# Kernel tuning notes

Hardware: AMD Instinct MI355X
Metric: run time of the kernel (lower is better)

## Reference

```python
import jax, jax.numpy as jnp
import numpy as np

N_NODES = 50000
N_EDGES = 800000
IN_FEATURES = 256
HIDDEN = 128


def setup_inputs() -> dict:
    key = jax.random.key(0)
    k_x, k_r, k_c, k_v, k_w, k_b = jax.random.split(key, 6)
    x = jax.random.normal(k_x, (N_NODES, IN_FEATURES), dtype=jnp.float32)
    adj_row = jax.random.randint(k_r, (N_EDGES,), 0, N_NODES, dtype=jnp.int32)
    adj_col = jax.random.randint(k_c, (N_EDGES,), 0, N_NODES, dtype=jnp.int32)
    adj_val = jax.random.uniform(k_v, (N_EDGES,), dtype=jnp.float32)
    # Linear params: weight [hidden, in_features] (xavier-normal-ish), bias [hidden]
    std = float(np.sqrt(2.0 / (IN_FEATURES + HIDDEN)))
    W = jax.random.normal(k_w, (HIDDEN, IN_FEATURES), dtype=jnp.float32) * std
    b = jax.random.normal(k_b, (HIDDEN,), dtype=jnp.float32) * 0.01
    return {"x": x, "adj_row": adj_row, "adj_col": adj_col, "adj_val": adj_val, "W": W, "b": b}


def reference(x, adj_row, adj_col, adj_val, W, b):
    # support = Linear(x): [N, hidden]
    support = jnp.einsum('nf,hf->nh', x, W) + b
    # sparse adj @ support via edge-list gather + segment-sum scatter
    gathered = support[adj_col] * adj_val[:, None]          # [E, hidden]
    out = jax.ops.segment_sum(gathered, adj_row, num_segments=N_NODES)  # [N, hidden]
    return out
```

## Files before the change

kernel.cpp:

```cpp
#include <hip/hip_runtime.h>

#define N_NODES 50000
#define N_EDGES 800000
#define IN_F    256
#define HIDDEN  128

#define BUCKET_SZ 64
#define NB        782
#define NBINS     1024
#define EBLOCK    3328
#define EPT       13
#define EBLOCKS   241
#define LIN_ROWS  64
#define LBLOCKS   782
#define NTASKS    1023
#define OFST_W    256
#define CAP       1300
#define NFRAG     4096

#define SMEM_BYTES 35840

typedef __attribute__((ext_vector_type(8))) short bf16x8;
typedef __attribute__((ext_vector_type(4))) float f32x4;

__device__ inline unsigned short f2bf(float f) {
    unsigned u = __float_as_uint(f);
    u += 0x7FFF + ((u >> 16) & 1);
    return (unsigned short)(u >> 16);
}
__device__ inline bf16x8 cvt8(float4 a, float4 b) {
    bf16x8 r;
    r[0] = (short)f2bf(a.x); r[1] = (short)f2bf(a.y);
    r[2] = (short)f2bf(a.z); r[3] = (short)f2bf(a.w);
    r[4] = (short)f2bf(b.x); r[5] = (short)f2bf(b.y);
    r[6] = (short)f2bf(b.z); r[7] = (short)f2bf(b.w);
    return r;
}
__device__ inline float bfLo(unsigned u) { return __uint_as_float(u << 16); }
__device__ inline float bfHi(unsigned u) { return __uint_as_float(u & 0xFFFF0000u); }

__global__ __launch_bounds__(256) void wconv_kernel(
    const float* __restrict__ W, unsigned short* __restrict__ wb)
{
    const int f = blockIdx.x * 256 + threadIdx.x;
    if (f >= NFRAG) return;
    const int ln = f & 63;
    const int s  = (f >> 6) & 7;
    const int hk = f >> 9;
    const int row = s * 16 + (ln & 15);
    const int k0  = hk * 32 + (ln >> 4) * 8;
    const float* wp = W + (size_t)row * IN_F + k0;
    float4 b0 = *(const float4*)wp;
    float4 b1 = *(const float4*)(wp + 4);
    *(bf16x8*)(wb + (size_t)f * 8) = cvt8(b0, b1);
}

__global__ __launch_bounds__(256, 4) void fused_linear_partition_kernel(
    const float* __restrict__ x, const unsigned short* __restrict__ wb,
    const float* __restrict__ bias, unsigned short* __restrict__ support,
    const int* __restrict__ adj_row, const int* __restrict__ adj_col,
    const float* __restrict__ adj_val,
    int2* __restrict__ part, int* __restrict__ ofsT)
{
    const int tid = threadIdx.x;

    if (blockIdx.x < EBLOCKS) {
        __shared__ __align__(16) char smem[SMEM_BYTES];
        int2* lbuf = (int2*)smem;
        int*  lofs = (int*)(smem + 26624);
        int*  lcur = (int*)(smem + 30720);
        int*  tsum = (int*)(smem + 34816);

        const int task = blockIdx.x;
        const int base = task * EBLOCK;
        const int n    = min(EBLOCK, N_EDGES - base);

        for (int i = tid; i < NBINS; i += 256) lofs[i] = 0;
        __syncthreads();

        unsigned pk[EPT]; float pv[EPT];
#pragma unroll
        for (int i = 0; i < EPT; ++i) {
            int li = tid + i * 256;
            bool ok = li < n;
            int ee = ok ? (base + li) : base;
            int r = adj_row[ee], c = adj_col[ee];
            float v = adj_val[ee];
            if (ok) {
                unsigned bk = (unsigned)r >> 6;
                pk[i] = (bk << 22) | (((unsigned)r & 63u) << 16) | (unsigned)c;
                pv[i] = v;
                atomicAdd(&lofs[bk], 1);
            } else pk[i] = 0xFFFFFFFFu;
        }
        __syncthreads();

        int s0 = lofs[tid * 4], s1 = lofs[tid * 4 + 1];
        int s2 = lofs[tid * 4 + 2], s3 = lofs[tid * 4 + 3];
        int mysum = s0 + s1 + s2 + s3;
        tsum[tid] = mysum;
        __syncthreads();
#pragma unroll
        for (int off = 1; off < 256; off <<= 1) {
            int t = (tid >= off) ? tsum[tid - off] : 0;
            __syncthreads();
            tsum[tid] += t;
            __syncthreads();
        }
        int ex = tsum[tid] - mysum;
        lofs[tid * 4]     = ex;
        lofs[tid * 4 + 1] = ex + s0;
        lofs[tid * 4 + 2] = ex + s0 + s1;
        lofs[tid * 4 + 3] = ex + s0 + s1 + s2;
        __syncthreads();

        for (int i = tid; i < NBINS; i += 256) lcur[i] = lofs[i];
        __syncthreads();

#pragma unroll
        for (int i = 0; i < EPT; ++i) {
            if (pk[i] != 0xFFFFFFFFu) {
                unsigned bk = pk[i] >> 22;
                int p = atomicAdd(&lcur[bk], 1);
                lbuf[p] = make_int2((int)(pk[i] & 0x3FFFFF), __float_as_int(pv[i]));
            }
        }
        __syncthreads();

        for (int j = tid; j < n; j += 256)
            part[(size_t)task * EBLOCK + j] = lbuf[j];
        for (int i = tid; i <= NB; i += 256)
            ofsT[(size_t)i * OFST_W + task] = lofs[i];
    } else {
        const int bid  = blockIdx.x - EBLOCKS;
        const int lane = tid & 63;
        const int wave = tid >> 6;
        const int quad = lane >> 4;
        const int l16  = lane & 15;

        int m = bid * LIN_ROWS + wave * 16 + l16;
        if (m >= N_NODES) m = N_NODES - 1;
        const float* xrow = x + (size_t)m * IN_F;
        const bf16x8* wbv = (const bf16x8*)wb;

        f32x4 acc[8];
#pragma unroll
        for (int s = 0; s < 8; ++s) acc[s] = (f32x4){0.f, 0.f, 0.f, 0.f};

#pragma unroll 2
        for (int hk = 0; hk < 8; ++hk) {
            const int k0 = hk * 32 + quad * 8;
            float4 a0 = *(const float4*)(xrow + k0);
            float4 a1 = *(const float4*)(xrow + k0 + 4);
            bf16x8 af = cvt8(a0, a1);
            const bf16x8* bb = wbv + (size_t)hk * 512 + lane;
#pragma unroll
            for (int s = 0; s < 8; ++s) {
                bf16x8 bf = bb[(size_t)s * 64];
                acc[s] = __builtin_amdgcn_mfma_f32_16x16x32_bf16(af, bf, acc[s], 0, 0, 0);
            }
        }

        const int rowBase = bid * LIN_ROWS + wave * 16 + quad * 4;
#pragma unroll
        for (int reg = 0; reg < 4; ++reg) {
            const int r = rowBase + reg;
            if (r < N_NODES) {
#pragma unroll
                for (int s = 0; s < 8; ++s) {
                    const int col = s * 16 + l16;
                    float v = acc[s][reg] + bias[col];
                    support[(size_t)r * HIDDEN + col] = f2bf(v);
                }
            }
        }
    }
}

__global__ __launch_bounds__(512) void bucket_gather_kernel(
    const int* __restrict__ ofsT, const int2* __restrict__ part,
    const unsigned int* __restrict__ support_u32, float* __restrict__ out)
{
    __shared__ int2 sbufA[CAP];
    __shared__ int2 sbufB[CAP];
    __shared__ int  wsum[8];
    __shared__ int  hist[BUCKET_SZ];
    __shared__ int  rp[BUCKET_SZ + 1];
    __shared__ int  cur[BUCKET_SZ];

    const int tid  = threadIdx.x;
    const int b    = blockIdx.x;
    const int wave = tid >> 6;
    const int lane = tid & 63;

    if (tid < BUCKET_SZ) hist[tid] = 0;

    int s0 = 0, slen = 0;
    if (tid < EBLOCKS) {
        s0   = ofsT[(size_t)b * OFST_W + tid];
        slen = ofsT[(size_t)(b + 1) * OFST_W + tid] - s0;
    }

    int iv = slen;
#pragma unroll
    for (int off = 1; off < 64; off <<= 1) {
        int t = __shfl_up(iv, off);
        if (lane >= off) iv += t;
    }
    if (lane == 63) wsum[wave] = iv;
    __syncthreads();
    int wpre = 0, total = 0;
#pragma unroll
    for (int w = 0; w < 8; ++w) {
        int sw = wsum[w];
        total += sw;
        if (w < wave) wpre += sw;
    }
    const int excl = wpre + iv - slen;
    const int n    = min(total, CAP);

    {
        const int2* seg = part + (size_t)tid * EBLOCK + s0;
        for (int k = 0; k < slen; ++k) {
            int p = excl + k;
            if (p < CAP) {
                int2 cv = seg[k];
                sbufA[p] = cv;
                atomicAdd(&hist[(cv.x >> 16) & 63], 1);
            }
        }
    }
    __syncthreads();

    if (tid < 64) {
        int a = hist[tid];
        int ia = a;
#pragma unroll
        for (int off = 1; off < 64; off <<= 1) {
            int t = __shfl_up(ia, off);
            if (tid >= off) ia += t;
        }
        rp[tid + 1] = ia;
        if (tid == 0) rp[0] = 0;
        cur[tid] = ia - a;
    }
    __syncthreads();

    for (int j = tid; j < n; j += 512) {
        int2 cv = sbufA[j];
        int p = atomicAdd(&cur[(cv.x >> 16) & 63], 1);
        sbufB[p] = cv;
    }
    __syncthreads();

    const int q   = lane >> 4;
    const int l16 = lane & 15;
    const uint4* support4 = (const uint4*)support_u32;
    const int rowLo = wave * 8;
#pragma unroll 1
    for (int r = rowLo; r < rowLo + 8; ++r) {
        const int grow = b * BUCKET_SZ + r;
        if (grow >= N_NODES) break;
        const int s = rp[r], e = rp[r + 1];
        float a0 = 0.f, a1 = 0.f, a2 = 0.f, a3 = 0.f;
        float a4 = 0.f, a5 = 0.f, a6 = 0.f, a7 = 0.f;
        for (int j = s; j < e; j += 8) {
            int iA  = j + q;
            int icA = min(iA, e - 1);
            int2 cA = sbufB[icA];
            float vA = (iA < e) ? __int_as_float(cA.y) : 0.f;
            uint4 uA = support4[(size_t)(cA.x & 0xFFFF) * 16 + l16];
            int iB  = j + 4 + q;
            int icB = min(iB, e - 1);
            int2 cB = sbufB[icB];
            float vB = (iB < e) ? __int_as_float(cB.y) : 0.f;
            uint4 uB = support4[(size_t)(cB.x & 0xFFFF) * 16 + l16];

            a0 += vA * bfLo(uA.x); a1 += vA * bfHi(uA.x);
            a2 += vA * bfLo(uA.y); a3 += vA * bfHi(uA.y);
            a4 += vA * bfLo(uA.z); a5 += vA * bfHi(uA.z);
            a6 += vA * bfLo(uA.w); a7 += vA * bfHi(uA.w);
            a0 += vB * bfLo(uB.x); a1 += vB * bfHi(uB.x);
            a2 += vB * bfLo(uB.y); a3 += vB * bfHi(uB.y);
            a4 += vB * bfLo(uB.z); a5 += vB * bfHi(uB.z);
            a6 += vB * bfLo(uB.w); a7 += vB * bfHi(uB.w);
        }
        a0 += __shfl_xor(a0, 16); a0 += __shfl_xor(a0, 32);
        a1 += __shfl_xor(a1, 16); a1 += __shfl_xor(a1, 32);
        a2 += __shfl_xor(a2, 16); a2 += __shfl_xor(a2, 32);
        a3 += __shfl_xor(a3, 16); a3 += __shfl_xor(a3, 32);
        a4 += __shfl_xor(a4, 16); a4 += __shfl_xor(a4, 32);
        a5 += __shfl_xor(a5, 16); a5 += __shfl_xor(a5, 32);
        a6 += __shfl_xor(a6, 16); a6 += __shfl_xor(a6, 32);
        a7 += __shfl_xor(a7, 16); a7 += __shfl_xor(a7, 32);
        float s0v, s1v;
        if      (q == 0) { s0v = a0; s1v = a1; }
        else if (q == 1) { s0v = a2; s1v = a3; }
        else if (q == 2) { s0v = a4; s1v = a5; }
        else             { s0v = a6; s1v = a7; }
        *(float2*)(out + (size_t)grow * HIDDEN + l16 * 8 + q * 2) = make_float2(s0v, s1v);
    }
}

extern "C" void kernel_launch(void* const* d_in, const int* in_sizes, int n_in,
                              void* d_out, int out_size, void* d_ws, size_t ws_size,
                              hipStream_t stream) {
    const float* x       = (const float*)d_in[0];
    const int*   adj_row = (const int*)d_in[1];
    const int*   adj_col = (const int*)d_in[2];
    const float* adj_val = (const float*)d_in[3];
    const float* W       = (const float*)d_in[4];
    const float* b       = (const float*)d_in[5];
    float* out = (float*)d_out;

    char* wsb = (char*)d_ws;
    const size_t off_support = 0;
    const size_t off_part    = off_support + (size_t)N_NODES * HIDDEN * 2;
    const size_t off_ofsT    = off_part + (size_t)EBLOCKS * EBLOCK * 8;
    const size_t off_wb      = off_ofsT + (size_t)(NB + 1) * OFST_W * 4;

    unsigned short* support = (unsigned short*)(wsb + off_support);
    int2* part = (int2*)(wsb + off_part);
    int*  ofsT = (int*)(wsb + off_ofsT);
    unsigned short* wb = (unsigned short*)(wsb + off_wb);

    wconv_kernel<<<NFRAG / 256, 256, 0, stream>>>(W, wb);
    fused_linear_partition_kernel<<<NTASKS, 256, 0, stream>>>(
        x, wb, b, support, adj_row, adj_col, adj_val, part, ofsT);
    bucket_gather_kernel<<<NB, 512, 0, stream>>>(
        ofsT, part, (const unsigned int*)support, out);
}
```

Baseline: 155.9 us.

## Replace two-level bucket partition with per-row atomic slot buffers plus overflow spill

The block-local bucket sort with prefix scans and the per-bucket shared-memory re-sort are replaced by a global atomic counter per destination row that writes each edge into a fixed 64-slot row buffer. Edges beyond 64 for a row go to an overflow list handled by a single-block atomic fixup kernel. The gather kernel then reads each row's slots directly with 16 lanes per row and no shared memory or shuffles. This trades scans and sorting for 800K global atomics, a memset, a padded slot buffer that scatters writes, and overflow capacity limits (OV_CAP) that could drop edges on skewed graphs.

```diff
diff --git a/kernel.cpp b/kernel.cpp
--- a/kernel.cpp
+++ b/kernel.cpp
@@ -5,20 +5,16 @@
 #define IN_F    256
 #define HIDDEN  128
 
-#define BUCKET_SZ 64
-#define NB        782
-#define NBINS     1024
-#define EBLOCK    3328
-#define EPT       13
-#define EBLOCKS   241
+#define EBLOCK    2048
+#define EBLOCKS   391
 #define LIN_ROWS  64
 #define LBLOCKS   782
-#define NTASKS    1023
-#define OFST_W    256
-#define CAP       1300
+#define NTASKS    1173
+#define SLOTS     64
+#define OV_CAP    4096
 #define NFRAG     4096
-
-#define SMEM_BYTES 35840
+#define GROWS     32
+#define GBLOCKS   1563
 
 typedef __attribute__((ext_vector_type(8))) short bf16x8;
 typedef __attribute__((ext_vector_type(4))) float f32x4;
@@ -60,77 +56,28 @@
     const float* __restrict__ bias, unsigned short* __restrict__ support,
     const int* __restrict__ adj_row, const int* __restrict__ adj_col,
     const float* __restrict__ adj_val,
-    int2* __restrict__ part, int* __restrict__ ofsT)
+    int2* __restrict__ slotbuf, int* __restrict__ cnt,
+    int4* __restrict__ ovbuf, int* __restrict__ ovcnt)
 {
     const int tid = threadIdx.x;
 
     if (blockIdx.x < EBLOCKS) {
-        __shared__ __align__(16) char smem[SMEM_BYTES];
-        int2* lbuf = (int2*)smem;
-        int*  lofs = (int*)(smem + 26624);
-        int*  lcur = (int*)(smem + 30720);
-        int*  tsum = (int*)(smem + 34816);
-
-        const int task = blockIdx.x;
-        const int base = task * EBLOCK;
-        const int n    = min(EBLOCK, N_EDGES - base);
-
-        for (int i = tid; i < NBINS; i += 256) lofs[i] = 0;
-        __syncthreads();
-
-        unsigned pk[EPT]; float pv[EPT];
-#pragma unroll
-        for (int i = 0; i < EPT; ++i) {
-            int li = tid + i * 256;
-            bool ok = li < n;
-            int ee = ok ? (base + li) : base;
-            int r = adj_row[ee], c = adj_col[ee];
-            float v = adj_val[ee];
-            if (ok) {
-                unsigned bk = (unsigned)r >> 6;
-                pk[i] = (bk << 22) | (((unsigned)r & 63u) << 16) | (unsigned)c;
-                pv[i] = v;
-                atomicAdd(&lofs[bk], 1);
-            } else pk[i] = 0xFFFFFFFFu;
-        }
-        __syncthreads();
-
-        int s0 = lofs[tid * 4], s1 = lofs[tid * 4 + 1];
-        int s2 = lofs[tid * 4 + 2], s3 = lofs[tid * 4 + 3];
-        int mysum = s0 + s1 + s2 + s3;
-        tsum[tid] = mysum;
-        __syncthreads();
-#pragma unroll
-        for (int off = 1; off < 256; off <<= 1) {
-            int t = (tid >= off) ? tsum[tid - off] : 0;
-            __syncthreads();
-            tsum[tid] += t;
-            __syncthreads();
-        }
-        int ex = tsum[tid] - mysum;
-        lofs[tid * 4]     = ex;
-        lofs[tid * 4 + 1] = ex + s0;
-        lofs[tid * 4 + 2] = ex + s0 + s1;
-        lofs[tid * 4 + 3] = ex + s0 + s1 + s2;
-        __syncthreads();
-
-        for (int i = tid; i < NBINS; i += 256) lcur[i] = lofs[i];
-        __syncthreads();
-
-#pragma unroll
-        for (int i = 0; i < EPT; ++i) {
-            if (pk[i] != 0xFFFFFFFFu) {
-                unsigned bk = pk[i] >> 22;
-                int p = atomicAdd(&lcur[bk], 1);
-                lbuf[p] = make_int2((int)(pk[i] & 0x3FFFFF), __float_as_int(pv[i]));
+        const int base = blockIdx.x * EBLOCK;
+#pragma unroll
+        for (int i = 0; i < 8; ++i) {
+            int e = base + tid + i * 256;
+            if (e < N_EDGES) {
+                int r = adj_row[e], c = adj_col[e];
+                float v = adj_val[e];
+                int pos = atomicAdd(&cnt[r], 1);
+                if (pos < SLOTS) {
+                    slotbuf[(size_t)r * SLOTS + pos] = make_int2(c, __float_as_int(v));
+                } else {
+                    int op = atomicAdd(ovcnt, 1);
+                    if (op < OV_CAP) ovbuf[op] = make_int4(r, c, __float_as_int(v), 0);
+                }
             }
         }
-        __syncthreads();
-
-        for (int j = tid; j < n; j += 256)
-            part[(size_t)task * EBLOCK + j] = lbuf[j];
-        for (int i = tid; i <= NB; i += 256)
-            ofsT[(size_t)i * OFST_W + task] = lofs[i];
     } else {
         const int bid  = blockIdx.x - EBLOCKS;
         const int lane = tid & 63;
@@ -177,128 +124,77 @@
     }
 }
 
-__global__ __launch_bounds__(512) void bucket_gather_kernel(
-    const int* __restrict__ ofsT, const int2* __restrict__ part,
+__global__ __launch_bounds__(512) void csr_gather_kernel(
+    const int* __restrict__ cnt, const int2* __restrict__ slotbuf,
     const unsigned int* __restrict__ support_u32, float* __restrict__ out)
 {
-    __shared__ int2 sbufA[CAP];
-    __shared__ int2 sbufB[CAP];
-    __shared__ int  wsum[8];
-    __shared__ int  hist[BUCKET_SZ];
-    __shared__ int  rp[BUCKET_SZ + 1];
-    __shared__ int  cur[BUCKET_SZ];
-
-    const int tid  = threadIdx.x;
-    const int b    = blockIdx.x;
-    const int wave = tid >> 6;
-    const int lane = tid & 63;
-
-    if (tid < BUCKET_SZ) hist[tid] = 0;
-
-    int s0 = 0, slen = 0;
-    if (tid < EBLOCKS) {
-        s0   = ofsT[(size_t)b * OFST_W + tid];
-        slen = ofsT[(size_t)(b + 1) * OFST_W + tid] - s0;
+    const int tid = threadIdx.x;
+    const int qw  = tid >> 4;
+    const int l16 = tid & 15;
+    const int row = blockIdx.x * GROWS + qw;
+    if (row >= N_NODES) return;
+
+    const int nc = min(cnt[row], SLOTS);
+    const int2* sl = slotbuf + (size_t)row * SLOTS;
+    const uint4* support4 = (const uint4*)support_u32;
+
+    float a0 = 0.f, a1 = 0.f, a2 = 0.f, a3 = 0.f;
+    float a4 = 0.f, a5 = 0.f, a6 = 0.f, a7 = 0.f;
+
+    for (int j = 0; j < nc; j += 4) {
+        int iA = j,     icA = min(iA, nc - 1);
+        int iB = j + 1, icB = min(iB, nc - 1);
+        int iC = j + 2, icC = min(iC, nc - 1);
+        int iD = j + 3, icD = min(iD, nc - 1);
+        int2 cA = sl[icA];
+        int2 cB = sl[icB];
+        int2 cC = sl[icC];
+        int2 cD = sl[icD];
+        float vA = (iA < nc) ? __int_as_float(cA.y) : 0.f;
+        float vB = (iB < nc) ? __int_as_float(cB.y) : 0.f;
+        float vC = (iC < nc) ? __int_as_float(cC.y) : 0.f;
+        float vD = (iD < nc) ? __int_as_float(cD.y) : 0.f;
+        uint4 uA = support4[(size_t)cA.x * 16 + l16];
+        uint4 uB = support4[(size_t)cB.x * 16 + l16];
+        uint4 uC = support4[(size_t)cC.x * 16 + l16];
+        uint4 uD = support4[(size_t)cD.x * 16 + l16];
+
+        a0 += vA * bfLo(uA.x); a1 += vA * bfHi(uA.x);
+        a2 += vA * bfLo(uA.y); a3 += vA * bfHi(uA.y);
+        a4 += vA * bfLo(uA.z); a5 += vA * bfHi(uA.z);
+        a6 += vA * bfLo(uA.w); a7 += vA * bfHi(uA.w);
+        a0 += vB * bfLo(uB.x); a1 += vB * bfHi(uB.x);
+        a2 += vB * bfLo(uB.y); a3 += vB * bfHi(uB.y);
+        a4 += vB * bfLo(uB.z); a5 += vB * bfHi(uB.z);
+        a6 += vB * bfLo(uB.w); a7 += vB * bfHi(uB.w);
+        a0 += vC * bfLo(uC.x); a1 += vC * bfHi(uC.x);
+        a2 += vC * bfLo(uC.y); a3 += vC * bfHi(uC.y);
+        a4 += vC * bfLo(uC.z); a5 += vC * bfHi(uC.z);
+        a6 += vC * bfLo(uC.w); a7 += vC * bfHi(uC.w);
+        a0 += vD * bfLo(uD.x); a1 += vD * bfHi(uD.x);
+        a2 += vD * bfLo(uD.y); a3 += vD * bfHi(uD.y);
+        a4 += vD * bfLo(uD.z); a5 += vD * bfHi(uD.z);
+        a6 += vD * bfLo(uD.w); a7 += vD * bfHi(uD.w);
     }
 
-    int iv = slen;
-#pragma unroll
-    for (int off = 1; off < 64; off <<= 1) {
-        int t = __shfl_up(iv, off);
-        if (lane >= off) iv += t;
-    }
-    if (lane == 63) wsum[wave] = iv;
-    __syncthreads();
-    int wpre = 0, total = 0;
-#pragma unroll
-    for (int w = 0; w < 8; ++w) {
-        int sw = wsum[w];
-        total += sw;
-        if (w < wave) wpre += sw;
-    }
-    const int excl = wpre + iv - slen;
-    const int n    = min(total, CAP);
-
-    {
-        const int2* seg = part + (size_t)tid * EBLOCK + s0;
-        for (int k = 0; k < slen; ++k) {
-            int p = excl + k;
-            if (p < CAP) {
-                int2 cv = seg[k];
-                sbufA[p] = cv;
-                atomicAdd(&hist[(cv.x >> 16) & 63], 1);
-            }
-        }
-    }
-    __syncthreads();
-
-    if (tid < 64) {
-        int a = hist[tid];
-        int ia = a;
-#pragma unroll
-        for (int off = 1; off < 64; off <<= 1) {
-            int t = __shfl_up(ia, off);
-            if (tid >= off) ia += t;
-        }
-        rp[tid + 1] = ia;
-        if (tid == 0) rp[0] = 0;
-        cur[tid] = ia - a;
-    }
-    __syncthreads();
-
-    for (int j = tid; j < n; j += 512) {
-        int2 cv = sbufA[j];
-        int p = atomicAdd(&cur[(cv.x >> 16) & 63], 1);
-        sbufB[p] = cv;
-    }
-    __syncthreads();
-
-    const int q   = lane >> 4;
-    const int l16 = lane & 15;
-    const uint4* support4 = (const uint4*)support_u32;
-    const int rowLo = wave * 8;
-#pragma unroll 1
-    for (int r = rowLo; r < rowLo + 8; ++r) {
-        const int grow = b * BUCKET_SZ + r;
-        if (grow >= N_NODES) break;
-        const int s = rp[r], e = rp[r + 1];
-        float a0 = 0.f, a1 = 0.f, a2 = 0.f, a3 = 0.f;
-        float a4 = 0.f, a5 = 0.f, a6 = 0.f, a7 = 0.f;
-        for (int j = s; j < e; j += 8) {
-            int iA  = j + q;
-            int icA = min(iA, e - 1);
-            int2 cA = sbufB[icA];
-            float vA = (iA < e) ? __int_as_float(cA.y) : 0.f;
-            uint4 uA = support4[(size_t)(cA.x & 0xFFFF) * 16 + l16];
-            int iB  = j + 4 + q;
-            int icB = min(iB, e - 1);
-            int2 cB = sbufB[icB];
-            float vB = (iB < e) ? __int_as_float(cB.y) : 0.f;
-            uint4 uB = support4[(size_t)(cB.x & 0xFFFF) * 16 + l16];
-
-            a0 += vA * bfLo(uA.x); a1 += vA * bfHi(uA.x);
-            a2 += vA * bfLo(uA.y); a3 += vA * bfHi(uA.y);
-            a4 += vA * bfLo(uA.z); a5 += vA * bfHi(uA.z);
-            a6 += vA * bfLo(uA.w); a7 += vA * bfHi(uA.w);
-            a0 += vB * bfLo(uB.x); a1 += vB * bfHi(uB.x);
-            a2 += vB * bfLo(uB.y); a3 += vB * bfHi(uB.y);
-            a4 += vB * bfLo(uB.z); a5 += vB * bfHi(uB.z);
-            a6 += vB * bfLo(uB.w); a7 += vB * bfHi(uB.w);
-        }
-        a0 += __shfl_xor(a0, 16); a0 += __shfl_xor(a0, 32);
-        a1 += __shfl_xor(a1, 16); a1 += __shfl_xor(a1, 32);
-        a2 += __shfl_xor(a2, 16); a2 += __shfl_xor(a2, 32);
-        a3 += __shfl_xor(a3, 16); a3 += __shfl_xor(a3, 32);
-        a4 += __shfl_xor(a4, 16); a4 += __shfl_xor(a4, 32);
-        a5 += __shfl_xor(a5, 16); a5 += __shfl_xor(a5, 32);
-        a6 += __shfl_xor(a6, 16); a6 += __shfl_xor(a6, 32);
-        a7 += __shfl_xor(a7, 16); a7 += __shfl_xor(a7, 32);
-        float s0v, s1v;
-        if      (q == 0) { s0v = a0; s1v = a1; }
-        else if (q == 1) { s0v = a2; s1v = a3; }
-        else if (q == 2) { s0v = a4; s1v = a5; }
-        else             { s0v = a6; s1v = a7; }
-        *(float2*)(out + (size_t)grow * HIDDEN + l16 * 8 + q * 2) = make_float2(s0v, s1v);
+    float* op = out + (size_t)row * HIDDEN + l16 * 8;
+    *(float4*)op       = make_float4(a0, a1, a2, a3);
+    *(float4*)(op + 4) = make_float4(a4, a5, a6, a7);
+}
+
+__global__ __launch_bounds__(256) void spill_fix_kernel(
+    const int* __restrict__ ovcnt, const int4* __restrict__ ovbuf,
+    const unsigned int* __restrict__ support_u32, float* __restrict__ out)
+{
+    const int n    = min(*ovcnt, OV_CAP);
+    const int wave = threadIdx.x >> 6;
+    const int lane = threadIdx.x & 63;
+    for (int j = wave; j < n; j += 4) {
+        int4 o = ovbuf[j];
+        unsigned u = support_u32[(size_t)o.y * 64 + lane];
+        float v = __int_as_float(o.z);
+        unsafeAtomicAdd(out + (size_t)o.x * HIDDEN + lane * 2,     v * bfLo(u));
+        unsafeAtomicAdd(out + (size_t)o.x * HIDDEN + lane * 2 + 1, v * bfHi(u));
     }
 }
 
@@ -315,18 +211,25 @@
 
     char* wsb = (char*)d_ws;
     const size_t off_support = 0;
-    const size_t off_part    = off_support + (size_t)N_NODES * HIDDEN * 2;
-    const size_t off_ofsT    = off_part + (size_t)EBLOCKS * EBLOCK * 8;
-    const size_t off_wb      = off_ofsT + (size_t)(NB + 1) * OFST_W * 4;
+    const size_t off_wb      = off_support + (size_t)N_NODES * HIDDEN * 2;
+    const size_t off_slot    = (off_wb + (size_t)NFRAG * 16 + 255) & ~(size_t)255;
+    const size_t off_cnt     = off_slot + (size_t)N_NODES * SLOTS * 8;
+    const size_t off_ovbuf   = (off_cnt + (size_t)(N_NODES + 1) * 4 + 15) & ~(size_t)15;
 
     unsigned short* support = (unsigned short*)(wsb + off_support);
-    int2* part = (int2*)(wsb + off_part);
-    int*  ofsT = (int*)(wsb + off_ofsT);
-    unsigned short* wb = (unsigned short*)(wsb + off_wb);
+    unsigned short* wb      = (unsigned short*)(wsb + off_wb);
+    int2* slotbuf = (int2*)(wsb + off_slot);
+    int*  cnt     = (int*)(wsb + off_cnt);
+    int*  ovcnt   = cnt + N_NODES;
+    int4* ovbuf   = (int4*)(wsb + off_ovbuf);
+
+    hipMemsetAsync(cnt, 0, (size_t)(N_NODES + 1) * 4, stream);
 
     wconv_kernel<<<NFRAG / 256, 256, 0, stream>>>(W, wb);
     fused_linear_partition_kernel<<<NTASKS, 256, 0, stream>>>(
-        x, wb, b, support, adj_row, adj_col, adj_val, part, ofsT);
-    bucket_gather_kernel<<<NB, 512, 0, stream>>>(
-        ofsT, part, (const unsigned int*)support, out);
-}
+        x, wb, b, support, adj_row, adj_col, adj_val, slotbuf, cnt, ovbuf, ovcnt);
+    csr_gather_kernel<<<GBLOCKS, 512, 0, stream>>>(
+        cnt, slotbuf, (const unsigned int*)support, out);
+    spill_fix_kernel<<<1, 256, 0, stream>>>(
+        ovcnt, ovbuf, (const unsigned int*)support, out);
+}
```

Measured after the change: 195.0 us. +25.1%, slower.
